# Optimization experiments

Measured on AMD Instinct MI355X. Metric: run time of the kernel, lower is better.

## Reference

```python
import jax, jax.numpy as jnp
import numpy as np


def _three_nn(xyz1, xyz2):
    # xyz1: [B,N1,3], xyz2: [B,N2,3]
    # Squared euclidean distances, as in the original three_nn CUDA/TF op.
    d2 = (jnp.sum(xyz1 * xyz1, axis=-1)[:, :, None]
          + jnp.sum(xyz2 * xyz2, axis=-1)[:, None, :]
          - 2.0 * jnp.einsum('bnd,bmd->bnm', xyz1, xyz2))  # [B,N1,N2]
    neg_vals, idx = jax.lax.top_k(-d2, 3)                 # 3 smallest
    return -neg_vals, idx                                  # dist [B,N1,3], idx [B,N1,3]


def reference(xyz1, xyz2, points1, points2, w1, w2):
    dist, idx = _three_nn(xyz1, xyz2)
    dist = jnp.maximum(dist, 1e-10)
    inv = 1.0 / dist                                       # [B,N1,3]
    weight = inv / jnp.sum(inv, axis=2, keepdims=True)     # [B,N1,3]

    B = points2.shape[0]
    b_idx = jnp.arange(B)[:, None, None]
    gathered = points2[b_idx, idx]                         # [B,N1,3,C2]
    interpolated = jnp.einsum('bnk,bnkc->bnc', weight, gathered)  # [B,N1,C2]

    new_points = jnp.concatenate([interpolated, points1], axis=2)  # [B,N1,C2+C1]

    # 1x1 conv MLP = per-point matmul; bn=False, activation=relu on all layers
    h = jax.nn.relu(jnp.einsum('bnc,cf->bnf', new_points, w1))
    h = jax.nn.relu(jnp.einsum('bnc,cf->bnf', h, w2))
    return h


def setup_inputs() -> dict:
    key = jax.random.key(0)
    k1, k2, k3, k4, k5, k6 = jax.random.split(key, 6)
    B, N1, N2, C1, C2 = 4, 8192, 2048, 128, 256
    xyz1 = jax.random.normal(k1, (B, N1, 3), dtype=jnp.float32)
    xyz2 = jax.random.normal(k2, (B, N2, 3), dtype=jnp.float32)
    points1 = jax.random.normal(k3, (B, N1, C1), dtype=jnp.float32)
    points2 = jax.random.normal(k4, (B, N2, C2), dtype=jnp.float32)
    # glorot-normal-ish init for the 1x1 conv kernels
    w1 = jax.random.normal(k5, (C2 + C1, 256), dtype=jnp.float32) * (2.0 / (C2 + C1 + 256)) ** 0.5
    w2 = jax.random.normal(k6, (256, 256), dtype=jnp.float32) * (2.0 / (256 + 256)) ** 0.5
    return {"xyz1": xyz1, "xyz2": xyz2, "points1": points1, "points2": points2, "w1": w1, "w2": w2}
```

## Files before the change

kernel.cpp:

```cpp
#include <hip/hip_runtime.h>
#include <stdint.h>

typedef unsigned short u16;
typedef unsigned int   u32;

#define NB 4
#define N1 8192
#define N2 2048
#define C1 128
#define C2 256
#define KK1 384
#define FF 256
#define TM 64
#define NTHR 1024
#define NCH 16
#define CHSZ (N2 / NCH)
#define TILES_PER_B (N1 / TM)
#define APAD 394
#define HPAD 266
#define NKT1 (KK1 / 32)
#define NKT2 (FF / 32)

typedef short short8 __attribute__((ext_vector_type(8)));
typedef float floatx4 __attribute__((ext_vector_type(4)));
typedef u32   u32x4  __attribute__((ext_vector_type(4)));

union ABFrag { u32 u[4]; short8 v; u32x4 q; };

__device__ __forceinline__ u16 f2b(float f) {
    u32 x = __float_as_uint(f);
    return (u16)((x + 0x7FFFu + ((x >> 16) & 1u)) >> 16);
}
__device__ __forceinline__ u32 pack2(float a, float b) {
    return (u32)f2b(a) | ((u32)f2b(b) << 16);
}

__global__ __launch_bounds__(256) void prep_kernel(
    const float* __restrict__ w1, const float* __restrict__ w2,
    const float* __restrict__ xyz2,
    u32x4* __restrict__ w1F, u32x4* __restrict__ w2F, float4* __restrict__ xp)
{
    int i = blockIdx.x * 256 + threadIdx.x;
    if (i < 16 * NKT1 * 64) {
        int nt = i / (NKT1 * 64), rem = i % (NKT1 * 64);
        int kt = rem / 64, lane = rem % 64;
        int n  = nt * 16 + (lane & 15);
        int k0 = kt * 32 + (lane >> 4) * 4;
        const float* wc = w1 + n;
        ABFrag f;
        f.u[0] = pack2(wc[(k0 + 0) * FF],  wc[(k0 + 1) * FF]);
        f.u[1] = pack2(wc[(k0 + 2) * FF],  wc[(k0 + 3) * FF]);
        f.u[2] = pack2(wc[(k0 + 16) * FF], wc[(k0 + 17) * FF]);
        f.u[3] = pack2(wc[(k0 + 18) * FF], wc[(k0 + 19) * FF]);
        w1F[i] = f.q;
        return;
    }
    i -= 16 * NKT1 * 64;
    if (i < 16 * NKT2 * 64) {
        int nt = i / (NKT2 * 64), rem = i % (NKT2 * 64);
        int kt = rem / 64, lane = rem % 64;
        int n  = nt * 16 + (lane & 15);
        int k0 = kt * 32 + (lane >> 4) * 4;
        const float* wc = w2 + n;
        ABFrag f;
        f.u[0] = pack2(wc[(k0 + 0) * FF],  wc[(k0 + 1) * FF]);
        f.u[1] = pack2(wc[(k0 + 2) * FF],  wc[(k0 + 3) * FF]);
        f.u[2] = pack2(wc[(k0 + 16) * FF], wc[(k0 + 17) * FF]);
        f.u[3] = pack2(wc[(k0 + 18) * FF], wc[(k0 + 19) * FF]);
        w2F[i] = f.q;
        return;
    }
    i -= 16 * NKT2 * 64;
    if (i < NB * N2) {
        const float* q = xyz2 + (size_t)i * 3;
        float x = q[0], y = q[1], z = q[2];
        float s2 = __fadd_rn(__fadd_rn(__fmul_rn(x,x), __fmul_rn(y,y)), __fmul_rn(z,z));
        xp[i] = make_float4(x, y, z, s2);
    }
}

__global__ __launch_bounds__(NTHR, 8) void fp_fused_kernel(
    const float* __restrict__ xyz1, const float* __restrict__ p1,
    const float* __restrict__ p2,
    const u32x4* __restrict__ w1F,  const u32x4* __restrict__ w2F,
    const float4* __restrict__ xp,  float* __restrict__ out)
{
    __shared__ int   s_idx[TM][3];
    __shared__ float s_wt[TM][3];
    __shared__ __align__(16) char s_buf[TM * APAD * 2];

    const int tid = threadIdx.x;
    const int b   = blockIdx.x / TILES_PER_B;
    const int t0  = (blockIdx.x % TILES_PER_B) * TM;

    float* pd = (float*)s_buf;
    int*   pi = (int*)(s_buf + NCH * TM * 3 * 4);

    {
        const int r  = tid & 63;
        const int ch = __builtin_amdgcn_readfirstlane(tid >> 6);
        const float4* cb = xp + (size_t)b * N2 + ch * CHSZ;
        const float* q = xyz1 + ((size_t)b * N1 + t0 + r) * 3;
        float qx = q[0], qy = q[1], qz = q[2];
        float s1 = __fadd_rn(__fadd_rn(__fmul_rn(qx,qx), __fmul_rn(qy,qy)), __fmul_rn(qz,qz));
        float bd0 = 3e38f, bd1 = 3e38f, bd2 = 3e38f;
        int   bi0 = 0, bi1 = 0, bi2 = 0;
        const int j0 = ch * CHSZ;
        #pragma unroll 8
        for (int jj = 0; jj < CHSZ; ++jj) {
            float4 p = cb[jj];
            float t  = __fadd_rn(__fadd_rn(__fmul_rn(qx,p.x), __fmul_rn(qy,p.y)), __fmul_rn(qz,p.z));
            float d  = __fsub_rn(__fadd_rn(s1, p.w), __fmul_rn(2.0f, t));
            float nb0 = fminf(d, bd0);
            float nb1 = __builtin_amdgcn_fmed3f(d, bd0, bd1);
            float nb2 = __builtin_amdgcn_fmed3f(d, bd1, bd2);
            bool c0 = d < bd0, c1 = d < bd1, c2 = d < bd2;
            int j  = j0 + jj;
            int t01 = c0 ? bi0 : j;
            bi0     = c0 ? j   : bi0;
            int t12 = c1 ? bi1 : j;
            bi1     = c1 ? t01 : bi1;
            bi2     = c2 ? t12 : bi2;
            bd0 = nb0; bd1 = nb1; bd2 = nb2;
        }
        const int o = (ch * TM + r) * 3;
        pd[o+0] = bd0; pd[o+1] = bd1; pd[o+2] = bd2;
        pi[o+0] = bi0; pi[o+1] = bi1; pi[o+2] = bi2;
    }
    __syncthreads();

    if (tid < TM) {
        float d0 = 3e38f, d1 = 3e38f, d2 = 3e38f;
        int   i0 = 0, i1 = 0, i2 = 0;
        for (int c = 0; c < NCH; ++c) {
            const int o = (c * TM + tid) * 3;
            #pragma unroll
            for (int k = 0; k < 3; ++k) {
                float d = pd[o + k]; int ix = pi[o + k];
                float n0 = fminf(d, d0);
                float n1 = __builtin_amdgcn_fmed3f(d, d0, d1);
                float n2 = __builtin_amdgcn_fmed3f(d, d1, d2);
                bool c0 = d < d0, c1 = d < d1, c2 = d < d2;
                int t01 = c0 ? i0 : ix;
                i0      = c0 ? ix : i0;
                int t12 = c1 ? i1 : t01;
                i1      = c1 ? t01 : i1;
                i2      = c2 ? t12 : i2;
                d0 = n0; d1 = n1; d2 = n2;
            }
        }
        d0 = fmaxf(d0, 1e-10f); d1 = fmaxf(d1, 1e-10f); d2 = fmaxf(d2, 1e-10f);
        float v0 = 1.0f / d0, v1 = 1.0f / d1, v2 = 1.0f / d2;
        float s  = 1.0f / (v0 + v1 + v2);
        s_wt[tid][0] = v0 * s; s_wt[tid][1] = v1 * s; s_wt[tid][2] = v2 * s;
        s_idx[tid][0] = i0; s_idx[tid][1] = i1; s_idx[tid][2] = i2;
    }
    __syncthreads();

    u16* A = (u16*)s_buf;
    {
        const float* pb = p2 + (size_t)b * N2 * C2;
        const int col2 = (tid & 127) * 2;
        for (int rr = (tid >> 7); rr < TM; rr += 8) {
            float w0 = s_wt[rr][0], w1v = s_wt[rr][1], w2v = s_wt[rr][2];
            int   i0 = s_idx[rr][0], i1 = s_idx[rr][1], i2 = s_idx[rr][2];
            float2 a0 = *(const float2*)(pb + (size_t)i0 * C2 + col2);
            float2 a1 = *(const float2*)(pb + (size_t)i1 * C2 + col2);
            float2 a2 = *(const float2*)(pb + (size_t)i2 * C2 + col2);
            float e0 = w0 * a0.x + w1v * a1.x + w2v * a2.x;
            float e1 = w0 * a0.y + w1v * a1.y + w2v * a2.y;
            *(u32*)(A + rr * APAD + col2) = pack2(e0, e1);
        }
        const int c4 = (tid & 31) * 4, r32 = tid >> 5;
        #pragma unroll
        for (int rv = 0; rv < 2; ++rv) {
            int rr = r32 + rv * 32;
            float4 v = *(const float4*)(p1 + ((size_t)b * N1 + t0 + rr) * C1 + c4);
            u32* w = (u32*)(A + rr * APAD + 256 + c4);
            w[0] = pack2(v.x, v.y);
            w[1] = pack2(v.z, v.w);
        }
    }
    __syncthreads();

    const int lane = tid & 63;
    const int wv   = tid >> 6;
    const int lr   = lane & 15;
    const int lg   = lane >> 4;
    const int lk   = lg << 2;
    const int wvb  = wv * 16;

    int id1[4], id2[4];
    {
        u16 rbf = f2b((float)lr);
        u16 c32 = f2b(1.0f / 32.0f);
        ABFrag pa, pc;
        u32 ra = (u32)rbf | ((u32)rbf << 16);
        u32 rc = (u32)c32 | ((u32)c32 << 16);
        pa.u[0] = pa.u[1] = pa.u[2] = pa.u[3] = ra;
        pc.u[0] = pc.u[1] = pc.u[2] = pc.u[3] = rc;
        floatx4 z = {0.f, 0.f, 0.f, 0.f};
        floatx4 D1 = __builtin_amdgcn_mfma_f32_16x16x32_bf16(pa.v, pc.v, z, 0, 0, 0);
        floatx4 D2 = __builtin_amdgcn_mfma_f32_16x16x32_bf16(pc.v, pa.v, z, 0, 0, 0);
        #pragma unroll
        for (int g = 0; g < 4; ++g) { id1[g] = (int)(D1[g] + 0.5f); id2[g] = (int)(D2[g] + 0.5f); }
    }

    floatx4 acc[4];
    #pragma unroll
    for (int i = 0; i < 4; ++i) acc[i] = floatx4{0.f, 0.f, 0.f, 0.f};

    {
        const u32x4* wf = w1F + (size_t)(wv * NKT1) * 64 + lane;
        for (int kk = 0; kk < NKT1; ++kk) {
            const int kb = kk * 32 + lk;
            ABFrag bf; bf.q = wf[(size_t)kk * 64];
            ABFrag a[4];
            #pragma unroll
            for (int rt = 0; rt < 4; ++rt) {
                const u32* ap = (const u32*)(A + (rt * 16 + lr) * APAD + kb);
                a[rt].u[0] = ap[0]; a[rt].u[1] = ap[1];
                a[rt].u[2] = ap[8]; a[rt].u[3] = ap[9];
            }
            #pragma unroll
            for (int rt = 0; rt < 4; ++rt)
                acc[rt] = __builtin_amdgcn_mfma_f32_16x16x32_bf16(a[rt].v, bf.v, acc[rt], 0, 0, 0);
        }
    }
    __syncthreads();

    u16* H = (u16*)s_buf;
    #pragma unroll
    for (int rt = 0; rt < 4; ++rt)
        #pragma unroll
        for (int g = 0; g < 4; ++g) {
            int row = rt * 16 + id1[g];
            int col = wvb + id2[g];
            H[row * HPAD + col] = f2b(fmaxf(acc[rt][g], 0.0f));
        }
    __syncthreads();

    floatx4 acc2[4];
    #pragma unroll
    for (int i = 0; i < 4; ++i) acc2[i] = floatx4{0.f, 0.f, 0.f, 0.f};

    {
        const u32x4* wf = w2F + (size_t)(wv * NKT2) * 64 + lane;
        for (int kk = 0; kk < NKT2; ++kk) {
            const int kb = kk * 32 + lk;
            ABFrag bf; bf.q = wf[(size_t)kk * 64];
            ABFrag a[4];
            #pragma unroll
            for (int rt = 0; rt < 4; ++rt) {
                const u32* ap = (const u32*)(H + (rt * 16 + lr) * HPAD + kb);
                a[rt].u[0] = ap[0]; a[rt].u[1] = ap[1];
                a[rt].u[2] = ap[8]; a[rt].u[3] = ap[9];
            }
            #pragma unroll
            for (int rt = 0; rt < 4; ++rt)
                acc2[rt] = __builtin_amdgcn_mfma_f32_16x16x32_bf16(a[rt].v, bf.v, acc2[rt], 0, 0, 0);
        }
    }

    float* ob = out + ((size_t)b * N1 + t0) * FF;
    #pragma unroll
    for (int rt = 0; rt < 4; ++rt)
        #pragma unroll
        for (int g = 0; g < 4; ++g) {
            int row = rt * 16 + id1[g];
            int col = wvb + id2[g];
            ob[(size_t)row * FF + col] = fmaxf(acc2[rt][g], 0.0f);
        }
}

extern "C" void kernel_launch(void* const* d_in, const int* in_sizes, int n_in,
                              void* d_out, int out_size, void* d_ws, size_t ws_size,
                              hipStream_t stream)
{
    (void)in_sizes; (void)n_in; (void)out_size; (void)ws_size;
    const float* xyz1 = (const float*)d_in[0];
    const float* xyz2 = (const float*)d_in[1];
    const float* p1   = (const float*)d_in[2];
    const float* p2   = (const float*)d_in[3];
    const float* w1   = (const float*)d_in[4];
    const float* w2   = (const float*)d_in[5];
    float* out = (float*)d_out;

    u32x4*  w1F = (u32x4*)d_ws;
    u32x4*  w2F = w1F + 16 * NKT1 * 64;
    float4* xpw = (float4*)(w2F + 16 * NKT2 * 64);

    int prep_items = 16 * NKT1 * 64 + 16 * NKT2 * 64 + NB * N2;
    prep_kernel<<<(prep_items + 255) / 256, 256, 0, stream>>>(w1, w2, xyz2, w1F, w2F, xpw);
    fp_fused_kernel<<<NB * TILES_PER_B, NTHR, 0, stream>>>(xyz1, p1, p2, w1F, w2F, xpw, out);
}
```

Before: 70.69 us.

## Pair candidate points for packed-math NN search and use 128-bit LDS fragment loads

Candidate xyz2 points are stored in pairs with a pre-scaled -2x layout so two distances are computed with packed float2 math. The bf16 weight fragments are repacked with 8 contiguous k values per lane, and the LDS row pads are widened so A/H fragments can be read with single 128-bit loads. The points1 copy is moved ahead of the NN search into a separate LDS region so its global loads overlap that phase, and the points2 gather is vectorized to float4. LDS use grows, which may reduce occupancy, and the reordered K mapping and distance arithmetic must still match the reference within tolerance.

```diff
diff --git a/kernel.cpp b/kernel.cpp
--- a/kernel.cpp
+++ b/kernel.cpp
@@ -16,13 +16,17 @@
 #define NCH 16
 #define CHSZ (N2 / NCH)
 #define TILES_PER_B (N1 / TM)
-#define APAD 394
-#define HPAD 266
+#define APAD 400
+#define HPAD 272
 #define NKT1 (KK1 / 32)
 #define NKT2 (FF / 32)
+#define ABYTES (TM * APAD * 2)
+#define PDOFF  ABYTES
+#define PIOFF  (ABYTES + NCH * TM * 3 * 4)
 
 typedef short short8 __attribute__((ext_vector_type(8)));
 typedef float floatx4 __attribute__((ext_vector_type(4)));
+typedef float f32x2  __attribute__((ext_vector_type(2)));
 typedef u32   u32x4  __attribute__((ext_vector_type(4)));
 
 union ABFrag { u32 u[4]; short8 v; u32x4 q; };
@@ -38,20 +42,20 @@
 __global__ __launch_bounds__(256) void prep_kernel(
     const float* __restrict__ w1, const float* __restrict__ w2,
     const float* __restrict__ xyz2,
-    u32x4* __restrict__ w1F, u32x4* __restrict__ w2F, float4* __restrict__ xp)
+    u32x4* __restrict__ w1F, u32x4* __restrict__ w2F, float* __restrict__ xq)
 {
     int i = blockIdx.x * 256 + threadIdx.x;
     if (i < 16 * NKT1 * 64) {
         int nt = i / (NKT1 * 64), rem = i % (NKT1 * 64);
         int kt = rem / 64, lane = rem % 64;
         int n  = nt * 16 + (lane & 15);
-        int k0 = kt * 32 + (lane >> 4) * 4;
+        int k0 = kt * 32 + (lane >> 4) * 8;
         const float* wc = w1 + n;
         ABFrag f;
-        f.u[0] = pack2(wc[(k0 + 0) * FF],  wc[(k0 + 1) * FF]);
-        f.u[1] = pack2(wc[(k0 + 2) * FF],  wc[(k0 + 3) * FF]);
-        f.u[2] = pack2(wc[(k0 + 16) * FF], wc[(k0 + 17) * FF]);
-        f.u[3] = pack2(wc[(k0 + 18) * FF], wc[(k0 + 19) * FF]);
+        f.u[0] = pack2(wc[(k0 + 0) * FF], wc[(k0 + 1) * FF]);
+        f.u[1] = pack2(wc[(k0 + 2) * FF], wc[(k0 + 3) * FF]);
+        f.u[2] = pack2(wc[(k0 + 4) * FF], wc[(k0 + 5) * FF]);
+        f.u[3] = pack2(wc[(k0 + 6) * FF], wc[(k0 + 7) * FF]);
         w1F[i] = f.q;
         return;
     }
@@ -60,13 +64,13 @@
         int nt = i / (NKT2 * 64), rem = i % (NKT2 * 64);
         int kt = rem / 64, lane = rem % 64;
         int n  = nt * 16 + (lane & 15);
-        int k0 = kt * 32 + (lane >> 4) * 4;
+        int k0 = kt * 32 + (lane >> 4) * 8;
         const float* wc = w2 + n;
         ABFrag f;
-        f.u[0] = pack2(wc[(k0 + 0) * FF],  wc[(k0 + 1) * FF]);
-        f.u[1] = pack2(wc[(k0 + 2) * FF],  wc[(k0 + 3) * FF]);
-        f.u[2] = pack2(wc[(k0 + 16) * FF], wc[(k0 + 17) * FF]);
-        f.u[3] = pack2(wc[(k0 + 18) * FF], wc[(k0 + 19) * FF]);
+        f.u[0] = pack2(wc[(k0 + 0) * FF], wc[(k0 + 1) * FF]);
+        f.u[1] = pack2(wc[(k0 + 2) * FF], wc[(k0 + 3) * FF]);
+        f.u[2] = pack2(wc[(k0 + 4) * FF], wc[(k0 + 5) * FF]);
+        f.u[3] = pack2(wc[(k0 + 6) * FF], wc[(k0 + 7) * FF]);
         w2F[i] = f.q;
         return;
     }
@@ -75,7 +79,12 @@
         const float* q = xyz2 + (size_t)i * 3;
         float x = q[0], y = q[1], z = q[2];
         float s2 = __fadd_rn(__fadd_rn(__fmul_rn(x,x), __fmul_rn(y,y)), __fmul_rn(z,z));
-        xp[i] = make_float4(x, y, z, s2);
+        int p = i >> 1, e = i & 1;
+        float* rec = xq + (size_t)p * 8;
+        rec[0 + e] = -2.0f * x;
+        rec[2 + e] = -2.0f * y;
+        rec[4 + e] = -2.0f * z;
+        rec[6 + e] = s2;
     }
 }
 
@@ -83,45 +92,75 @@
     const float* __restrict__ xyz1, const float* __restrict__ p1,
     const float* __restrict__ p2,
     const u32x4* __restrict__ w1F,  const u32x4* __restrict__ w2F,
-    const float4* __restrict__ xp,  float* __restrict__ out)
+    const float4* __restrict__ xq,  float* __restrict__ out)
 {
     __shared__ int   s_idx[TM][3];
     __shared__ float s_wt[TM][3];
-    __shared__ __align__(16) char s_buf[TM * APAD * 2];
+    __shared__ __align__(16) char s_buf[ABYTES + NCH * TM * 3 * 8];
 
     const int tid = threadIdx.x;
     const int b   = blockIdx.x / TILES_PER_B;
     const int t0  = (blockIdx.x % TILES_PER_B) * TM;
 
-    float* pd = (float*)s_buf;
-    int*   pi = (int*)(s_buf + NCH * TM * 3 * 4);
+    u16*   A  = (u16*)s_buf;
+    float* pd = (float*)(s_buf + PDOFF);
+    int*   pi = (int*)(s_buf + PIOFF);
+
+    {
+        const int c4 = (tid & 31) * 4, r32 = tid >> 5;
+        #pragma unroll
+        for (int rv = 0; rv < 2; ++rv) {
+            int rr = r32 + rv * 32;
+            float4 v = *(const float4*)(p1 + ((size_t)b * N1 + t0 + rr) * C1 + c4);
+            u32* w = (u32*)(A + rr * APAD + 256 + c4);
+            w[0] = pack2(v.x, v.y);
+            w[1] = pack2(v.z, v.w);
+        }
+    }
 
     {
         const int r  = tid & 63;
         const int ch = __builtin_amdgcn_readfirstlane(tid >> 6);
-        const float4* cb = xp + (size_t)b * N2 + ch * CHSZ;
+        const float4* cb = xq + ((size_t)b * (N2 / 2) + ch * (CHSZ / 2)) * 2;
         const float* q = xyz1 + ((size_t)b * N1 + t0 + r) * 3;
         float qx = q[0], qy = q[1], qz = q[2];
         float s1 = __fadd_rn(__fadd_rn(__fmul_rn(qx,qx), __fmul_rn(qy,qy)), __fmul_rn(qz,qz));
         float bd0 = 3e38f, bd1 = 3e38f, bd2 = 3e38f;
         int   bi0 = 0, bi1 = 0, bi2 = 0;
         const int j0 = ch * CHSZ;
-        #pragma unroll 8
-        for (int jj = 0; jj < CHSZ; ++jj) {
-            float4 p = cb[jj];
-            float t  = __fadd_rn(__fadd_rn(__fmul_rn(qx,p.x), __fmul_rn(qy,p.y)), __fmul_rn(qz,p.z));
-            float d  = __fsub_rn(__fadd_rn(s1, p.w), __fmul_rn(2.0f, t));
-            float nb0 = fminf(d, bd0);
-            float nb1 = __builtin_amdgcn_fmed3f(d, bd0, bd1);
-            float nb2 = __builtin_amdgcn_fmed3f(d, bd1, bd2);
-            bool c0 = d < bd0, c1 = d < bd1, c2 = d < bd2;
-            int j  = j0 + jj;
-            int t01 = c0 ? bi0 : j;
-            bi0     = c0 ? j   : bi0;
-            int t12 = c1 ? bi1 : j;
-            bi1     = c1 ? t01 : bi1;
-            bi2     = c2 ? t12 : bi2;
-            bd0 = nb0; bd1 = nb1; bd2 = nb2;
+        #pragma unroll 4
+        for (int jj = 0; jj < CHSZ / 2; ++jj) {
+            float4 f0 = cb[2 * jj];
+            float4 f1 = cb[2 * jj + 1];
+            f32x2 dpair;
+            {
+                #pragma clang fp contract(off)
+                f32x2 qx2 = {qx, qx}, qy2 = {qy, qy}, qz2 = {qz, qz}, s1v = {s1, s1};
+                f32x2 nx = {f0.x, f0.y}, ny = {f0.z, f0.w};
+                f32x2 nz = {f1.x, f1.y}, ss = {f1.z, f1.w};
+                f32x2 u  = qx2 * nx;
+                f32x2 v  = qy2 * ny;
+                f32x2 w  = u + v;
+                f32x2 z2 = qz2 * nz;
+                f32x2 t  = w + z2;
+                f32x2 s12 = s1v + ss;
+                dpair = s12 + t;
+            }
+            #pragma unroll
+            for (int e = 0; e < 2; ++e) {
+                float d = dpair[e];
+                int   j = j0 + 2 * jj + e;
+                float nb0 = fminf(d, bd0);
+                float nb1 = __builtin_amdgcn_fmed3f(d, bd0, bd1);
+                float nb2 = __builtin_amdgcn_fmed3f(d, bd1, bd2);
+                bool c0 = d < bd0, c1 = d < bd1, c2 = d < bd2;
+                int t01 = c0 ? bi0 : j;
+                bi0     = c0 ? j   : bi0;
+                int t12 = c1 ? bi1 : j;
+                bi1     = c1 ? t01 : bi1;
+                bi2     = c2 ? t12 : bi2;
+                bd0 = nb0; bd1 = nb1; bd2 = nb2;
+            }
         }
         const int o = (ch * TM + r) * 3;
         pd[o+0] = bd0; pd[o+1] = bd1; pd[o+2] = bd2;
@@ -157,28 +196,25 @@
     }
     __syncthreads();
 
-    u16* A = (u16*)s_buf;
     {
         const float* pb = p2 + (size_t)b * N2 * C2;
-        const int col2 = (tid & 127) * 2;
-        for (int rr = (tid >> 7); rr < TM; rr += 8) {
+        const int col4 = (tid & 63) * 4;
+        const int wvr  = tid >> 6;
+        #pragma unroll
+        for (int m = 0; m < 4; ++m) {
+            int rr = wvr + m * 16;
             float w0 = s_wt[rr][0], w1v = s_wt[rr][1], w2v = s_wt[rr][2];
             int   i0 = s_idx[rr][0], i1 = s_idx[rr][1], i2 = s_idx[rr][2];
-            float2 a0 = *(const float2*)(pb + (size_t)i0 * C2 + col2);
-            float2 a1 = *(const float2*)(pb + (size_t)i1 * C2 + col2);
-            float2 a2 = *(const float2*)(pb + (size_t)i2 * C2 + col2);
+            float4 a0 = *(const float4*)(pb + (size_t)i0 * C2 + col4);
+            float4 a1 = *(const float4*)(pb + (size_t)i1 * C2 + col4);
+            float4 a2 = *(const float4*)(pb + (size_t)i2 * C2 + col4);
             float e0 = w0 * a0.x + w1v * a1.x + w2v * a2.x;
             float e1 = w0 * a0.y + w1v * a1.y + w2v * a2.y;
-            *(u32*)(A + rr * APAD + col2) = pack2(e0, e1);
-        }
-        const int c4 = (tid & 31) * 4, r32 = tid >> 5;
-        #pragma unroll
-        for (int rv = 0; rv < 2; ++rv) {
-            int rr = r32 + rv * 32;
-            float4 v = *(const float4*)(p1 + ((size_t)b * N1 + t0 + rr) * C1 + c4);
-            u32* w = (u32*)(A + rr * APAD + 256 + c4);
-            w[0] = pack2(v.x, v.y);
-            w[1] = pack2(v.z, v.w);
+            float e2 = w0 * a0.z + w1v * a1.z + w2v * a2.z;
+            float e3 = w0 * a0.w + w1v * a1.w + w2v * a2.w;
+            u32* w = (u32*)(A + rr * APAD + col4);
+            w[0] = pack2(e0, e1);
+            w[1] = pack2(e2, e3);
         }
     }
     __syncthreads();
@@ -187,7 +223,6 @@
     const int wv   = tid >> 6;
     const int lr   = lane & 15;
     const int lg   = lane >> 4;
-    const int lk   = lg << 2;
     const int wvb  = wv * 16;
 
     int id1[4], id2[4];
@@ -212,16 +247,13 @@
 
     {
         const u32x4* wf = w1F + (size_t)(wv * NKT1) * 64 + lane;
+        const int kb8 = lg * 8;
         for (int kk = 0; kk < NKT1; ++kk) {
-            const int kb = kk * 32 + lk;
             ABFrag bf; bf.q = wf[(size_t)kk * 64];
             ABFrag a[4];
             #pragma unroll
-            for (int rt = 0; rt < 4; ++rt) {
-                const u32* ap = (const u32*)(A + (rt * 16 + lr) * APAD + kb);
-                a[rt].u[0] = ap[0]; a[rt].u[1] = ap[1];
-                a[rt].u[2] = ap[8]; a[rt].u[3] = ap[9];
-            }
+            for (int rt = 0; rt < 4; ++rt)
+                a[rt].q = *(const u32x4*)(A + (rt * 16 + lr) * APAD + kk * 32 + kb8);
             #pragma unroll
             for (int rt = 0; rt < 4; ++rt)
                 acc[rt] = __builtin_amdgcn_mfma_f32_16x16x32_bf16(a[rt].v, bf.v, acc[rt], 0, 0, 0);
@@ -246,16 +278,13 @@
 
     {
         const u32x4* wf = w2F + (size_t)(wv * NKT2) * 64 + lane;
+        const int kb8 = lg * 8;
         for (int kk = 0; kk < NKT2; ++kk) {
-            const int kb = kk * 32 + lk;
             ABFrag bf; bf.q = wf[(size_t)kk * 64];
             ABFrag a[4];
             #pragma unroll
-            for (int rt = 0; rt < 4; ++rt) {
-                const u32* ap = (const u32*)(H + (rt * 16 + lr) * HPAD + kb);
-                a[rt].u[0] = ap[0]; a[rt].u[1] = ap[1];
-                a[rt].u[2] = ap[8]; a[rt].u[3] = ap[9];
-            }
+            for (int rt = 0; rt < 4; ++rt)
+                a[rt].q = *(const u32x4*)(H + (rt * 16 + lr) * HPAD + kk * 32 + kb8);
             #pragma unroll
             for (int rt = 0; rt < 4; ++rt)
                 acc2[rt] = __builtin_amdgcn_mfma_f32_16x16x32_bf16(a[rt].v, bf.v, acc2[rt], 0, 0, 0);
@@ -286,11 +315,12 @@
     const float* w2   = (const float*)d_in[5];
     float* out = (float*)d_out;
 
-    u32x4*  w1F = (u32x4*)d_ws;
-    u32x4*  w2F = w1F + 16 * NKT1 * 64;
-    float4* xpw = (float4*)(w2F + 16 * NKT2 * 64);
+    u32x4* w1F = (u32x4*)d_ws;
+    u32x4* w2F = w1F + 16 * NKT1 * 64;
+    float* xqw = (float*)(w2F + 16 * NKT2 * 64);
 
     int prep_items = 16 * NKT1 * 64 + 16 * NKT2 * 64 + NB * N2;
-    prep_kernel<<<(prep_items + 255) / 256, 256, 0, stream>>>(w1, w2, xyz2, w1F, w2F, xpw);
-    fp_fused_kernel<<<NB * TILES_PER_B, NTHR, 0, stream>>>(xyz1, p1, p2, w1F, w2F, xpw, out);
-}
+    prep_kernel<<<(prep_items + 255) / 256, 256, 0, stream>>>(w1, w2, xyz2, w1F, w2F, xqw);
+    fp_fused_kernel<<<NB * TILES_PER_B, NTHR, 0, stream>>>(
+        xyz1, p1, p2, w1F, w2F, (const float4*)xqw, out);
+}
```

After: 62.75 us. 1.13x faster.
